# Kernel tuning notes

Hardware: AMD Instinct MI355X
Metric: run time of the kernel (lower is better)

Reference implementation:

```python
import jax, jax.numpy as jnp
import numpy as np

LN_EPS = 1e-5

def _layernorm(x, w, b):
    mu = jnp.mean(x, axis=-1, keepdims=True)
    var = jnp.mean((x - mu) ** 2, axis=-1, keepdims=True)
    return (x - mu) * jax.lax.rsqrt(var + LN_EPS) * w + b

def _parallel_scan(A, B, x):
    # A, B, x: (Bb, L, S). Log-space cumsum trick, faithful to torch version.
    A_safe = jnp.clip(A, 0.001, 0.999)
    log_A = jnp.log(A_safe + 1e-10)
    log_cum_A = jnp.cumsum(log_A, axis=1)
    log_cum_A_max = jnp.max(log_cum_A, axis=1, keepdims=True)
    log_cum_A_c = log_cum_A - log_cum_A_max
    cum_A = jnp.exp(log_cum_A_c)
    BX = B * x
    # shifted (exclusive) centered log-cumsum: zeros at t=0
    zeros = jnp.zeros_like(log_cum_A_c[:, :1])
    log_cum_shift = jnp.concatenate([zeros, log_cum_A_c[:, :-1]], axis=1)
    BX_norm = BX * jnp.exp(-log_cum_shift)
    cum_BX = jnp.cumsum(BX_norm, axis=1)
    return cum_BX * cum_A

def setup_inputs() -> dict:
    key = jax.random.key(0)
    ks = jax.random.split(key, 8)
    Bb, L, D, S = 16, 4096, 512, 64
    def xavier(k, shape, gain):
        fan_out, fan_in = shape
        std = gain * np.sqrt(2.0 / (fan_in + fan_out))
        return jax.random.normal(k, shape, jnp.float32) * std
    x = jax.random.normal(ks[0], (Bb, L, D), jnp.float32)
    Wx = xavier(ks[1], (S, D), 0.5)
    Wdt = xavier(ks[2], (S, D), 1.0)
    WB = xavier(ks[3], (S, D), 0.4)
    WC = xavier(ks[4], (S, D), 0.4)
    Wout = xavier(ks[5], (D, S), 0.5)
    # A_init = -rand*0.8 - 0.2 ; A_log = log(-A_init) = log(uniform(0.2, 1.0))
    A_log = jnp.log(jax.random.uniform(ks[6], (S,), jnp.float32, 0.2, 1.0))
    return {
        "x": x,
        "ln_w": jnp.ones((D,), jnp.float32),
        "ln_b": jnp.zeros((D,), jnp.float32),
        "Wx": Wx, "bx": jnp.zeros((S,), jnp.float32),
        "Wdt": Wdt, "bdt": jnp.zeros((S,), jnp.float32),
        "A_log": A_log,
        "WB": WB, "WC": WC,
        "Dp": jnp.zeros((D,), jnp.float32),
        "Wout": Wout, "bout": jnp.zeros((D,), jnp.float32),
    }

def reference(x, ln_w, ln_b, Wx, bx, Wdt, bdt, A_log, WB, WC, Dp, Wout, bout):
    x_norm = _layernorm(x, ln_w, ln_b)                       # (B,L,D)
    delta = jax.nn.softplus(x_norm @ Wdt.T + bdt) * 0.01 + 0.0001  # (B,L,S)
    B_t = x_norm @ WB.T                                      # (B,L,S)
    C_t = x_norm @ WC.T                                      # (B,L,S)
    A = -jnp.exp(A_log)                                      # (S,)
    x_proj = x_norm @ Wx.T + bx                              # (B,L,S)
    deltaA = jnp.clip(delta * A, -10.0, -0.0001)
    A_disc = jnp.exp(deltaA)
    B_disc = delta * B_t
    h = _parallel_scan(A_disc, B_disc, x_proj)               # (B,L,S)
    y = C_t * h
    y = jnp.where(jnp.any(~jnp.isfinite(y)), jnp.zeros_like(y), y)
    y = y @ Wout.T + bout                                    # (B,L,D)
    D_safe = jnp.clip(Dp, -2.0, 2.0)
    return y + D_safe * x
```

## Files before the change

kernel.cpp:

```cpp
#include <hip/hip_runtime.h>
#include <hip/hip_bf16.h>
#include <math.h>

typedef __attribute__((ext_vector_type(4))) float  floatx4;
typedef __attribute__((ext_vector_type(8))) short  shortx8;
typedef unsigned short ushort_t;
typedef unsigned int   uint32;

#define BB 16
#define LL 4096
#define DD 512
#define SS 64
#define NTOK (BB*LL)
#define NCH 64

__device__ __forceinline__ ushort_t f2bf(float f) {
    uint32 u = __float_as_uint(f);
    u += 0x7FFFu + ((u >> 16) & 1u);
    return (ushort_t)(u >> 16);
}
__device__ __forceinline__ float bf2f(ushort_t u) {
    return __uint_as_float(((uint32)u) << 16);
}
__device__ __forceinline__ uint32 pack2(float lo, float hi) {
    __hip_bfloat162 h = __float22bfloat162_rn(make_float2(lo, hi));
    union { __hip_bfloat162 h; uint32 u; } cv; cv.h = h;
    return cv.u;
}

__device__ __forceinline__ void gload16(const void* g, void* l) {
    __builtin_amdgcn_global_load_lds(
        (const __attribute__((address_space(1))) unsigned int*)g,
        (__attribute__((address_space(3))) unsigned int*)l, 16, 0, 0);
}

__global__ __launch_bounds__(256) void k_prep(
    const float* __restrict__ Wdt, const float* __restrict__ WB,
    const float* __restrict__ WC,  const float* __restrict__ Wx,
    const float* __restrict__ Wout,
    const float* __restrict__ lnw, const float* __restrict__ lnb,
    ushort_t* __restrict__ wcat, ushort_t* __restrict__ woutb,
    float* __restrict__ u, float* __restrict__ c)
{
    const int bid = blockIdx.x;
    if (bid < 64) {
        const int wave = threadIdx.x >> 6, lane = threadIdx.x & 63;
        const int n = bid * 4 + wave;
        const float* src = (n < 64) ? Wdt : (n < 128) ? WB : (n < 192) ? WC : Wx;
        const float* row = src + (size_t)(n & 63) * 512;
        float4 a  = *(const float4*)(row + lane * 8);
        float4 b  = *(const float4*)(row + lane * 8 + 4);
        float4 wa = *(const float4*)(lnw + lane * 8);
        float4 wb = *(const float4*)(lnw + lane * 8 + 4);
        float4 ba = *(const float4*)(lnb + lane * 8);
        float4 bb = *(const float4*)(lnb + lane * 8 + 4);
        float w0 = a.x * wa.x, w1 = a.y * wa.y, w2 = a.z * wa.z, w3 = a.w * wa.w;
        float w4 = b.x * wb.x, w5 = b.y * wb.y, w6 = b.z * wb.z, w7 = b.w * wb.w;
        float us = w0 + w1 + w2 + w3 + w4 + w5 + w6 + w7;
        float cs = a.x*ba.x + a.y*ba.y + a.z*ba.z + a.w*ba.w
                 + b.x*bb.x + b.y*bb.y + b.z*bb.z + b.w*bb.w;
        uint4 o;
        o.x = (uint32)f2bf(w0) | ((uint32)f2bf(w1) << 16);
        o.y = (uint32)f2bf(w2) | ((uint32)f2bf(w3) << 16);
        o.z = (uint32)f2bf(w4) | ((uint32)f2bf(w5) << 16);
        o.w = (uint32)f2bf(w6) | ((uint32)f2bf(w7) << 16);
        ((uint4*)(wcat + (size_t)n * 512))[lane] = o;
        #pragma unroll
        for (int off = 32; off > 0; off >>= 1) {
            us += __shfl_xor(us, off);
            cs += __shfl_xor(cs, off);
        }
        if (lane == 0) { u[n] = us; c[n] = cs; }
    } else {
        int idx = (bid - 64) * 2048 + threadIdx.x * 8;
        float4 a = *(const float4*)(Wout + idx);
        float4 b = *(const float4*)(Wout + idx + 4);
        uint4 o;
        o.x = (uint32)f2bf(a.x) | ((uint32)f2bf(a.y) << 16);
        o.y = (uint32)f2bf(a.z) | ((uint32)f2bf(a.w) << 16);
        o.z = (uint32)f2bf(b.x) | ((uint32)f2bf(b.y) << 16);
        o.w = (uint32)f2bf(b.z) | ((uint32)f2bf(b.w) << 16);
        *(uint4*)(woutb + idx) = o;
    }
}

__global__ __launch_bounds__(512, 4) void k_proj(
    const float* __restrict__ x, const ushort_t* __restrict__ wcat,
    const float* __restrict__ u, const float* __restrict__ c,
    const float* __restrict__ bdt, const float* __restrict__ bx_, const float* __restrict__ A_log,
    float* __restrict__ Ap, float* __restrict__ BXv, ushort_t* __restrict__ Ctb,
    float* __restrict__ Asum, float* __restrict__ Bsum)
{
    __shared__ __align__(16) char sBuf[49152];
    __shared__ float sMu[128], sRs[128];
    ushort_t* sA = (ushort_t*)sBuf;
    ushort_t* sB = (ushort_t*)(sBuf + 16384);
    float*    sPA = (float*)sBuf;
    float*    sPB = sPA + 2 * 64 * 17;

    const int tid  = threadIdx.x;
    const int wave = tid >> 6, lane = tid & 63;
    const int ln   = lane & 15, qd = lane >> 4;
    const int mh   = wave >> 2, nq = wave & 3;
    const int token0 = blockIdx.x * 128;

    int tB[4], cB[4];
    #pragma unroll
    for (int r = 0; r < 4; r++) { int sl = r * 512 + tid; tB[r] = sl >> 3; cB[r] = ((sl & 7) ^ (tB[r] & 7)) * 8; }
    int rowA[2], k8A[2];
    #pragma unroll
    for (int r = 0; r < 2; r++) { int sl = r * 512 + tid; rowA[r] = sl >> 3; k8A[r] = sl & 7; }

    floatx4 acc[4][4] = {};
    float sacc[2] = {0.f, 0.f}, qacc[2] = {0.f, 0.f};

    for (int kc = 0; kc < 8; kc++) {
        const int kb = kc * 64;
        #pragma unroll
        for (int r = 0; r < 4; r++)
            gload16(wcat + (size_t)tB[r] * DD + kb + cB[r],
                    sBuf + 16384 + r * 8192 + wave * 1024);
        #pragma unroll
        for (int r = 0; r < 2; r++) {
            const float4* xp = (const float4*)(x + (size_t)(token0 + rowA[r]) * DD + kb + k8A[r] * 8);
            float4 v0 = xp[0], v1 = xp[1];
            sacc[r] += (v0.x + v0.y) + (v0.z + v0.w) + (v1.x + v1.y) + (v1.z + v1.w);
            qacc[r] += v0.x*v0.x + v0.y*v0.y + v0.z*v0.z + v0.w*v0.w
                     + v1.x*v1.x + v1.y*v1.y + v1.z*v1.z + v1.w*v1.w;
            uint4 pk;
            pk.x = pack2(v0.x, v0.y);
            pk.y = pack2(v0.z, v0.w);
            pk.z = pack2(v1.x, v1.y);
            pk.w = pack2(v1.z, v1.w);
            *(uint4*)(sBuf + rowA[r] * 128 + ((k8A[r] ^ (rowA[r] & 7)) << 4)) = pk;
        }
        __syncthreads();
        #pragma unroll
        for (int ks8 = 0; ks8 < 8; ks8 += 4) {
            shortx8 af[4], bf[4];
            #pragma unroll
            for (int mt = 0; mt < 4; mt++) {
                int t = mh * 64 + mt * 16 + ln;
                af[mt] = *(const shortx8*)&sA[t * 64 + (((ks8 + qd) ^ (ln & 7)) << 3)];
            }
            #pragma unroll
            for (int nt = 0; nt < 4; nt++) {
                int n = nt * 64 + nq * 16 + ln;
                bf[nt] = *(const shortx8*)&sB[n * 64 + (((ks8 + qd) ^ (ln & 7)) << 3)];
            }
            #pragma unroll
            for (int mt = 0; mt < 4; mt++)
                #pragma unroll
                for (int nt = 0; nt < 4; nt++)
                    acc[mt][nt] = __builtin_amdgcn_mfma_f32_16x16x32_bf16(
                        af[mt], bf[nt], acc[mt][nt], 0, 0, 0);
        }
        __syncthreads();
    }

    #pragma unroll
    for (int r = 0; r < 2; r++) {
        float s_ = sacc[r], q_ = qacc[r];
        s_ += __shfl_xor(s_, 1); q_ += __shfl_xor(q_, 1);
        s_ += __shfl_xor(s_, 2); q_ += __shfl_xor(q_, 2);
        s_ += __shfl_xor(s_, 4); q_ += __shfl_xor(q_, 4);
        if ((lane & 7) == 0) {
            int row = r * 64 + wave * 8 + (lane >> 3);
            float mu = s_ * (1.0f / 512.0f);
            sMu[row] = mu;
            sRs[row] = rsqrtf(q_ * (1.0f / 512.0f) - mu * mu + 1e-5f);
        }
    }
    __syncthreads();

    {
        const int s = nq * 16 + ln;
        float bdt_s = bdt[s], bx_s = bx_[s];
        float A_s = -expf(A_log[s]);
        float u0 = u[s], u1 = u[64 + s], u2 = u[128 + s], u3 = u[192 + s];
        float c0 = c[s], c1 = c[64 + s], c2 = c[128 + s], c3 = c[192 + s];
        const bool fc = ((blockIdx.x & 31) == 0) && (mh == 0);
        #pragma unroll
        for (int mt = 0; mt < 4; mt++) {
            float Al = 1.f, Bl = 0.f;
            #pragma unroll
            for (int r = 0; r < 4; r++) {
                int tl  = mt * 16 + qd * 4 + r;
                int tok = token0 + mh * 64 + tl;
                float mu_t = sMu[mh * 64 + tl], rs_t = sRs[mh * 64 + tl];
                float zdt = rs_t * (acc[mt][0][r] - mu_t * u0) + c0;
                float zb  = rs_t * (acc[mt][1][r] - mu_t * u1) + c1;
                float zc  = rs_t * (acc[mt][2][r] - mu_t * u2) + c2;
                float zx  = rs_t * (acc[mt][3][r] - mu_t * u3) + c3;
                float zin = zdt + bdt_s;
                float sp  = fmaxf(zin, 0.0f) + log1pf(expf(-fabsf(zin)));
                float delta = sp * 0.01f + 1e-4f;
                float dA    = fminf(fmaxf(delta * A_s, -10.0f), -1e-4f);
                float a     = fminf(fmaxf(expf(dA), 0.001f), 0.999f) + 1e-10f;
                float bxv   = delta * zb * (zx + bx_s);
                size_t g = (size_t)tok * 64 + s;
                Ap[g] = a; BXv[g] = bxv; Ctb[g] = f2bf(zc);
                bool first = fc && (tl == 0);
                float alpha = first ? 0.f : a;
                float beta  = first ? bxv : a * bxv;
                Al *= alpha;
                Bl = fmaf(alpha, Bl, beta);
            }
            sPA[(mh * 64 + s) * 17 + mt * 4 + qd] = Al;
            sPB[(mh * 64 + s) * 17 + mt * 4 + qd] = Bl;
        }
    }
    __syncthreads();
    if (tid < 128) {
        int ch = tid >> 6, ss = tid & 63;
        const float* pa = &sPA[(ch * 64 + ss) * 17];
        const float* pb = &sPB[(ch * 64 + ss) * 17];
        float A = pa[0], B = pb[0];
        #pragma unroll
        for (int g = 1; g < 16; g++) {
            A *= pa[g];
            B = fmaf(pa[g], B, pb[g]);
        }
        int o = (blockIdx.x * 2 + ch) * 64 + ss;
        Asum[o] = A; Bsum[o] = B;
    }
}

__global__ __launch_bounds__(256) void k_scan(
    const float* __restrict__ Ap, const float* __restrict__ BXv, const ushort_t* __restrict__ Ctb,
    const float* __restrict__ Asum, const float* __restrict__ Bsum,
    ushort_t* __restrict__ P)
{
    __shared__ float sAs[4096], sBs[4096];
    const int tid = threadIdx.x;
    const int b = blockIdx.x >> 4, cq = blockIdx.x & 15;
    #pragma unroll
    for (int i = 0; i < 16; i++) {
        int idx = i * 256 + tid;
        sAs[idx] = Asum[b * 4096 + idx];
        sBs[idx] = Bsum[b * 4096 + idx];
    }
    __syncthreads();
    const int w = tid >> 6, s = tid & 63;
    const int c = cq * 4 + w;
    float h = 0.f;
    for (int cc = 0; cc < c; cc++)
        h = fmaf(sAs[cc * 64 + s], h, sBs[cc * 64 + s]);
    size_t base = ((size_t)b * LL + c * 64) * 64 + s;
    const bool fc = (c == 0);
    #pragma unroll 8
    for (int t = 0; t < 64; t++) {
        float a = Ap[base + (size_t)t * 64];
        float v = BXv[base + (size_t)t * 64];
        float alpha = (fc && t == 0) ? 0.f : a;
        float beta  = (fc && t == 0) ? v   : a * v;
        h = fmaf(alpha, h, beta);
        P[base + (size_t)t * 64] = f2bf(bf2f(Ctb[base + (size_t)t * 64]) * h);
    }
}

__global__ __launch_bounds__(256, 4) void k_gemm2(
    const ushort_t* __restrict__ P, const ushort_t* __restrict__ woutb,
    const float* __restrict__ bout, const float* __restrict__ Dp,
    const float* __restrict__ x, float* __restrict__ out)
{
    __shared__ __align__(16) char sPBuf[8192];
    __shared__ __align__(16) float sOut[16 * 260];
    ushort_t* sP = (ushort_t*)sPBuf;

    const int tid  = threadIdx.x;
    const int wave = tid >> 6, lane = tid & 63;
    const int ln   = lane & 15, qd = lane >> 4;
    const int nq   = wave;
    const int token0 = blockIdx.x * 64;

    #pragma unroll
    for (int r = 0; r < 2; r++) {
        int sl = r * 256 + tid;
        int t = sl >> 3, k8 = (sl & 7) ^ (t & 7);
        gload16(P + (size_t)(token0 + t) * 64 + k8 * 8,
                sPBuf + r * 4096 + wave * 1024);
    }
    __syncthreads();

    #pragma unroll
    for (int half = 0; half < 2; half++) {
        const int nh = half * 256;
        floatx4 acc[4][4] = {};
        #pragma unroll
        for (int ks8 = 0; ks8 < 8; ks8 += 4) {
            shortx8 af[4], bf[4];
            #pragma unroll
            for (int mt = 0; mt < 4; mt++) {
                int t = mt * 16 + ln;
                af[mt] = *(const shortx8*)&sP[t * 64 + (((ks8 + qd) ^ (ln & 7)) << 3)];
            }
            #pragma unroll
            for (int nt = 0; nt < 4; nt++) {
                int d = nh + nq * 64 + nt * 16 + ln;
                bf[nt] = *(const shortx8*)(woutb + (size_t)d * 64 + (ks8 + qd) * 8);
            }
            #pragma unroll
            for (int mt = 0; mt < 4; mt++)
                #pragma unroll
                for (int nt = 0; nt < 4; nt++)
                    acc[mt][nt] = __builtin_amdgcn_mfma_f32_16x16x32_bf16(
                        af[mt], bf[nt], acc[mt][nt], 0, 0, 0);
        }

        for (int mt = 0; mt < 4; mt++) {
            __syncthreads();
            #pragma unroll
            for (int nt = 0; nt < 4; nt++)
                #pragma unroll
                for (int r = 0; r < 4; r++)
                    sOut[(qd * 4 + r) * 260 + nq * 64 + nt * 16 + ln] = acc[mt][nt][r];
            __syncthreads();
            #pragma unroll
            for (int i = 0; i < 4; i++) {
                int idx = i * 256 + tid;
                int row = idx >> 6, c4 = (idx & 63) * 4;
                int tok = token0 + mt * 16 + row;
                int d   = nh + c4;
                float4 o  = *(float4*)&sOut[row * 260 + c4];
                float4 xv = *(const float4*)(x + (size_t)tok * DD + d);
                float4 bo = *(const float4*)(bout + d);
                float4 dp = *(const float4*)(Dp + d);
                float4 res;
                res.x = fmaf(fminf(fmaxf(dp.x, -2.f), 2.f), xv.x, o.x + bo.x);
                res.y = fmaf(fminf(fmaxf(dp.y, -2.f), 2.f), xv.y, o.y + bo.y);
                res.z = fmaf(fminf(fmaxf(dp.z, -2.f), 2.f), xv.z, o.z + bo.z);
                res.w = fmaf(fminf(fmaxf(dp.w, -2.f), 2.f), xv.w, o.w + bo.w);
                *(float4*)(out + (size_t)tok * DD + d) = res;
            }
        }
    }
}

extern "C" void kernel_launch(void* const* d_in, const int* in_sizes, int n_in,
                              void* d_out, int out_size, void* d_ws, size_t ws_size,
                              hipStream_t stream)
{
    const float* x     = (const float*)d_in[0];
    const float* lnw   = (const float*)d_in[1];
    const float* lnb   = (const float*)d_in[2];
    const float* Wx    = (const float*)d_in[3];
    const float* bx_   = (const float*)d_in[4];
    const float* Wdt   = (const float*)d_in[5];
    const float* bdt   = (const float*)d_in[6];
    const float* A_log = (const float*)d_in[7];
    const float* WB    = (const float*)d_in[8];
    const float* WC    = (const float*)d_in[9];
    const float* Dp    = (const float*)d_in[10];
    const float* Wout  = (const float*)d_in[11];
    const float* bout  = (const float*)d_in[12];
    float* out = (float*)d_out;

    char* w = (char*)d_ws;
    constexpr size_t SZ_XN = (size_t)NTOK * DD * 2;
    constexpr size_t SZ_T  = (size_t)NTOK * 64 * 4;
    ushort_t* Pm    = (ushort_t*)(w);
    float*    Ap    = (float*)(w + SZ_XN);
    float*    BXv   = (float*)(w + SZ_XN + SZ_T);
    ushort_t* Ctb   = (ushort_t*)(w + SZ_XN + 2 * SZ_T);
    float*    Asum  = (float*)(w + SZ_XN + 3 * SZ_T);
    float*    Bsum  = (float*)(w + SZ_XN + 3 * SZ_T + 262144);
    ushort_t* Wcat  = (ushort_t*)(w + SZ_XN + 3 * SZ_T + 2 * 262144);
    ushort_t* WoutB = (ushort_t*)(w + SZ_XN + 3 * SZ_T + 2 * 262144 + 262144);
    float*    Uc    = (float*)(w + SZ_XN + 3 * SZ_T + 2 * 262144 + 262144 + 65536);
    float*    Cc    = Uc + 256;

    k_prep<<<80, 256, 0, stream>>>(Wdt, WB, WC, Wx, Wout, lnw, lnb, Wcat, WoutB, Uc, Cc);
    k_proj<<<NTOK / 128, 512, 0, stream>>>(x, Wcat, Uc, Cc, bdt, bx_, A_log,
                                           Ap, BXv, Ctb, Asum, Bsum);
    k_scan<<<BB * 16, 256, 0, stream>>>(Ap, BXv, Ctb, Asum, Bsum, Pm);
    k_gemm2<<<NTOK / 64, 256, 0, stream>>>(Pm, WoutB, bout, Dp, x, out);
}
```

Baseline: 343.4 us.

## Transpose output GEMM operands to write results directly, split D across blocks

The output projection now treats Wout rows as the MFMA A operand and tokens as B, so each lane's accumulator holds four consecutive D columns of one token. That lets it write float4 results straight to global memory, dropping the shared-memory staging buffer and its barriers. The D dimension is also split across two blocks, doubling the grid. The cost is that each P tile is loaded twice and the stores are less coalesced, with 16-byte chunks scattered across token rows.

New measurement: 354.1 us. 1.03x slower.

```diff
diff --git a/kernel.cpp b/kernel.cpp
--- a/kernel.cpp
+++ b/kernel.cpp
@@ -265,14 +265,13 @@
     const float* __restrict__ x, float* __restrict__ out)
 {
     __shared__ __align__(16) char sPBuf[8192];
-    __shared__ __align__(16) float sOut[16 * 260];
     ushort_t* sP = (ushort_t*)sPBuf;
 
     const int tid  = threadIdx.x;
     const int wave = tid >> 6, lane = tid & 63;
     const int ln   = lane & 15, qd = lane >> 4;
-    const int nq   = wave;
-    const int token0 = blockIdx.x * 64;
+    const int token0 = (blockIdx.x >> 1) * 64;
+    const int dw = (blockIdx.x & 1) * 256 + wave * 64;
 
     #pragma unroll
     for (int r = 0; r < 2; r++) {
@@ -283,56 +282,45 @@
     }
     __syncthreads();
 
-    #pragma unroll
-    for (int half = 0; half < 2; half++) {
-        const int nh = half * 256;
-        floatx4 acc[4][4] = {};
-        #pragma unroll
-        for (int ks8 = 0; ks8 < 8; ks8 += 4) {
-            shortx8 af[4], bf[4];
-            #pragma unroll
-            for (int mt = 0; mt < 4; mt++) {
-                int t = mt * 16 + ln;
-                af[mt] = *(const shortx8*)&sP[t * 64 + (((ks8 + qd) ^ (ln & 7)) << 3)];
-            }
-            #pragma unroll
-            for (int nt = 0; nt < 4; nt++) {
-                int d = nh + nq * 64 + nt * 16 + ln;
-                bf[nt] = *(const shortx8*)(woutb + (size_t)d * 64 + (ks8 + qd) * 8);
-            }
-            #pragma unroll
-            for (int mt = 0; mt < 4; mt++)
-                #pragma unroll
-                for (int nt = 0; nt < 4; nt++)
-                    acc[mt][nt] = __builtin_amdgcn_mfma_f32_16x16x32_bf16(
-                        af[mt], bf[nt], acc[mt][nt], 0, 0, 0);
-        }
-
+    floatx4 acc[4][4] = {};
+    #pragma unroll
+    for (int ks8 = 0; ks8 < 8; ks8 += 4) {
+        shortx8 af[4], bf[4];
+        #pragma unroll
         for (int mt = 0; mt < 4; mt++) {
-            __syncthreads();
+            int d = dw + mt * 16 + ln;
+            af[mt] = *(const shortx8*)(woutb + (size_t)d * 64 + (ks8 + qd) * 8);
+        }
+        #pragma unroll
+        for (int nt = 0; nt < 4; nt++) {
+            int t = nt * 16 + ln;
+            bf[nt] = *(const shortx8*)&sP[t * 64 + (((ks8 + qd) ^ (ln & 7)) << 3)];
+        }
+        #pragma unroll
+        for (int mt = 0; mt < 4; mt++)
             #pragma unroll
             for (int nt = 0; nt < 4; nt++)
-                #pragma unroll
-                for (int r = 0; r < 4; r++)
-                    sOut[(qd * 4 + r) * 260 + nq * 64 + nt * 16 + ln] = acc[mt][nt][r];
-            __syncthreads();
-            #pragma unroll
-            for (int i = 0; i < 4; i++) {
-                int idx = i * 256 + tid;
-                int row = idx >> 6, c4 = (idx & 63) * 4;
-                int tok = token0 + mt * 16 + row;
-                int d   = nh + c4;
-                float4 o  = *(float4*)&sOut[row * 260 + c4];
-                float4 xv = *(const float4*)(x + (size_t)tok * DD + d);
-                float4 bo = *(const float4*)(bout + d);
-                float4 dp = *(const float4*)(Dp + d);
-                float4 res;
-                res.x = fmaf(fminf(fmaxf(dp.x, -2.f), 2.f), xv.x, o.x + bo.x);
-                res.y = fmaf(fminf(fmaxf(dp.y, -2.f), 2.f), xv.y, o.y + bo.y);
-                res.z = fmaf(fminf(fmaxf(dp.z, -2.f), 2.f), xv.z, o.z + bo.z);
-                res.w = fmaf(fminf(fmaxf(dp.w, -2.f), 2.f), xv.w, o.w + bo.w);
-                *(float4*)(out + (size_t)tok * DD + d) = res;
-            }
+                acc[mt][nt] = __builtin_amdgcn_mfma_f32_16x16x32_bf16(
+                    af[mt], bf[nt], acc[mt][nt], 0, 0, 0);
+    }
+
+    #pragma unroll
+    for (int nt = 0; nt < 4; nt++) {
+        const int tok = token0 + nt * 16 + ln;
+        const float* xr = x + (size_t)tok * DD;
+        float* orow = out + (size_t)tok * DD;
+        #pragma unroll
+        for (int mt = 0; mt < 4; mt++) {
+            const int d0 = dw + mt * 16 + qd * 4;
+            float4 xv = *(const float4*)(xr + d0);
+            float4 bo = *(const float4*)(bout + d0);
+            float4 dp = *(const float4*)(Dp + d0);
+            float4 res;
+            res.x = fmaf(fminf(fmaxf(dp.x, -2.f), 2.f), xv.x, acc[mt][nt][0] + bo.x);
+            res.y = fmaf(fminf(fmaxf(dp.y, -2.f), 2.f), xv.y, acc[mt][nt][1] + bo.y);
+            res.z = fmaf(fminf(fmaxf(dp.z, -2.f), 2.f), xv.z, acc[mt][nt][2] + bo.z);
+            res.w = fmaf(fminf(fmaxf(dp.w, -2.f), 2.f), xv.w, acc[mt][nt][3] + bo.w);
+            *(float4*)(orow + d0) = res;
         }
     }
 }
@@ -374,5 +362,5 @@
     k_proj<<<NTOK / 128, 512, 0, stream>>>(x, Wcat, Uc, Cc, bdt, bx_, A_log,
                                            Ap, BXv, Ctb, Asum, Bsum);
     k_scan<<<BB * 16, 256, 0, stream>>>(Ap, BXv, Ctb, Asum, Bsum, Pm);
-    k_gemm2<<<NTOK / 64, 256, 0, stream>>>(Pm, WoutB, bout, Dp, x, out);
-}
+    k_gemm2<<<(NTOK / 64) * 2, 256, 0, stream>>>(Pm, WoutB, bout, Dp, x, out);
+}
```
